# Optimization experiments

Measured on AMD Instinct MI355X. Metric: run time of the kernel, lower is better.

The kernel has to match this reference:

```python
import jax, jax.numpy as jnp
import numpy as np

B, N, R, CIN = 2, 2048, 128, 256
RADIUS, NSAMPLE, OUT = 0.3, 16, 5
EPS = 1e-5


def setup_inputs():
    key = jax.random.key(0)
    ks = jax.random.split(key, 8)
    points_xyz = jax.random.uniform(ks[0], (B, N, 3)) * 2.0          # scene ~2m cube
    features = jax.random.normal(ks[1], (B, CIN, N))
    ctr = jax.random.uniform(ks[2], (B, R, 3)) * 2.0
    size = jax.random.uniform(ks[3], (B, R, 3)) * 0.6 + 0.3          # positive box sizes
    ang = jax.random.uniform(ks[4], (B, R, 1)) * np.pi
    rois = jnp.concatenate([ctr, size, ang], axis=-1)                # [B,R,7]
    s = 0.02
    W_mlp = jax.random.normal(ks[5], (256, CIN + 3)) * s
    g_mlp = jnp.ones((256,)); bt_mlp = jnp.zeros((256,))
    W1 = jax.random.normal(ks[6], (128, 256)) * s; b1 = jnp.zeros((128,))
    g1 = jnp.ones((128,)); bt1 = jnp.zeros((128,))
    W2 = jax.random.normal(ks[7], (128, 128)) * s; b2 = jnp.zeros((128,))
    g2 = jnp.ones((128,)); bt2 = jnp.zeros((128,))
    return dict(points_xyz=points_xyz, features=features, rois=rois,
                W_mlp=W_mlp, g_mlp=g_mlp, bt_mlp=bt_mlp,
                W1=W1, b1=b1, g1=g1, bt1=bt1,
                W2=W2, b2=b2, g2=g2, bt2=bt2)


def _bn(x, g, b, axes, shape):
    # training-mode BatchNorm (batch statistics), matching torch .train() forward
    m = jnp.mean(x, axes, keepdims=True)
    v = jnp.var(x, axes, keepdims=True)
    return (x - m) * jax.lax.rsqrt(v + EPS) * g.reshape(shape) + b.reshape(shape)


def _forward(points_xyz, features, rois, W_mlp, g_mlp, bt_mlp,
             W1, b1, g1, bt1, W2, b2, g2, bt2):
    # ---- QueryAndGroup: ball query (min_radius=0) + gather + center + normalize_xyz ----
    diff = points_xyz[:, :, None, :] - points_xyz[:, None, :, :]     # [B,Nq,Np,3]
    d2 = jnp.sum(diff * diff, -1)
    mask = d2 < RADIUS * RADIUS
    cand = jnp.where(mask, jnp.arange(N, dtype=jnp.int32)[None, None, :], N)
    idx = jnp.sort(cand, axis=-1)[..., :NSAMPLE]                     # first NSAMPLE in-ball, ascending point index
    idx = jnp.where(idx < N, idx, idx[..., :1])                      # pad with first valid (self always in-ball)
    gx = jax.vmap(lambda p, i: p[i])(points_xyz, idx)                # [B,N,S,3]
    gx = (gx - points_xyz[:, :, None, :]) / RADIUS                   # centered + normalized
    gf = jax.vmap(lambda f, i: f[i])(jnp.swapaxes(features, 1, 2), idx)  # [B,N,S,C]
    nf = jnp.transpose(jnp.concatenate([gx, gf], -1), (0, 3, 1, 2))  # [B,3+C,N,S] (use_xyz=True)
    # ---- mlp: Conv2d 1x1 (bias='auto' with BN -> no bias) + BN2d + ReLU ----
    h = jnp.einsum('oc,bcns->bons', W_mlp, nf)
    h = jax.nn.relu(_bn(h, g_mlp, bt_mlp, (0, 2, 3), (1, -1, 1, 1)))
    feats = jnp.max(h, -1)                                           # max_pool2d over samples -> [B,256,N]
    h = jnp.einsum('oc,bcn->bon', W1, feats) + b1[None, :, None]
    h = jax.nn.relu(_bn(h, g1, bt1, (0, 2), (1, -1, 1)))
    h = jnp.einsum('oc,bcn->bon', W2, h) + b2[None, :, None]
    feats = jax.nn.relu(_bn(h, g2, bt2, (0, 2), (1, -1, 1)))         # [B,128,N]
    # ---- RoIPool3d: roi-aware voxel max pool (out_size=5, mode='max') ----
    C = feats.shape[1]
    ctr, size, ry = rois[..., :3], rois[..., 3:6], rois[..., 6]
    rel = points_xyz[:, None, :, :] - ctr[:, :, None, :]             # [B,R,N,3]
    c = jnp.cos(ry)[:, :, None]; s = jnp.sin(ry)[:, :, None]
    lx = rel[..., 0] * c + rel[..., 1] * s                           # rotate by -ry into roi frame
    ly = -rel[..., 0] * s + rel[..., 1] * c
    local = jnp.stack([lx, ly, rel[..., 2]], -1)                     # [B,R,N,3]
    half = size[:, :, None, :] * 0.5
    inside = jnp.all(jnp.abs(local) < half, -1)                      # [B,R,N]
    v = jnp.clip(jnp.floor((local + half) / (2.0 * half) * OUT), 0, OUT - 1).astype(jnp.int32)
    vox = (v[..., 0] * OUT + v[..., 1]) * OUT + v[..., 2]
    base = jnp.arange(B * R, dtype=jnp.int32).reshape(B, R, 1) * (OUT ** 3)
    seg = jnp.where(inside, base + vox, B * R * OUT ** 3).reshape(-1)  # dummy segment for outside pts
    data = jnp.broadcast_to(jnp.swapaxes(feats, 1, 2)[:, None], (B, R, N, C)).reshape(-1, C)
    pooled = jax.ops.segment_max(data, seg, num_segments=B * R * OUT ** 3 + 1)[:-1]
    pooled = jnp.where(jnp.isneginf(pooled), 0.0, pooled)            # empty voxels -> 0
    roi_feats = pooled.reshape(B, R, OUT, OUT, OUT, C)
    return feats, roi_feats


def reference(points_xyz, features, rois, W_mlp, g_mlp, bt_mlp,
              W1, b1, g1, bt1, W2, b2, g2, bt2):
    return _forward(points_xyz, features, rois, W_mlp, g_mlp, bt_mlp,
                    W1, b1, g1, bt1, W2, b2, g2, bt2)
```

## Files before the change

kernel.cpp:

```cpp
#include <hip/hip_runtime.h>
#include <hip/hip_bf16.h>

typedef __hip_bfloat16 bf16;
typedef unsigned short u16;

#define NB   2
#define NPT  2048
#define NROI 128
#define CINF 256
#define NS   16
#define KDIM 259
#define KP2  288
#define C1   256
#define C2   128
#define NVOX 125
#define EPSF 1e-5f

typedef __bf16 bf16x8 __attribute__((ext_vector_type(8)));
typedef float  f32x4  __attribute__((ext_vector_type(4)));

__device__ __forceinline__ float ldin(const void* p, size_t i, int f32flag) {
    if (f32flag) return ((const float*)p)[i];
    unsigned short u = ((const unsigned short*)p)[i];
    return __uint_as_float(((unsigned)u) << 16);
}

__device__ __forceinline__ unsigned short f2bf(float x) {
    unsigned u = __float_as_uint(x);
    u += 0x7FFFu + ((u >> 16) & 1u);
    return (unsigned short)(u >> 16);
}


__global__ void k_detect(const void* __restrict__ Wm, int* __restrict__ flag) {
    __shared__ int f;
    int tid = threadIdx.x;
    if (tid == 0) f = 0;
    __syncthreads();
    #pragma unroll
    for (int r = 0; r < 4; r++) {
        unsigned short u = ((const unsigned short*)Wm)[r * 256 + tid];
        float v = __uint_as_float(((unsigned)u) << 16);
        if (!(fabsf(v) <= 1e4f)) atomicOr(&f, 1);
    }
    __syncthreads();
    if (tid == 0) *flag = f;
}

__global__ void k_cvt(const void* __restrict__ pts, const void* __restrict__ rois,
                      const void* __restrict__ gm, const void* __restrict__ btm,
                      const void* __restrict__ b1, const void* __restrict__ g1,
                      const void* __restrict__ bt1, const void* __restrict__ b2,
                      const void* __restrict__ g2, const void* __restrict__ bt2,
                      const void* __restrict__ Wm,
                      float* __restrict__ ptsf, float* __restrict__ roisf,
                      float* __restrict__ params, const int* __restrict__ flag) {
    int f = *flag;
    int e = blockIdx.x * 256 + threadIdx.x;
    if (blockIdx.y == 10) {
        if (e < 768) {
            int d = e >> 8, o = e & 255;
            params[25088 + e] = ldin(Wm, (size_t)o * KDIM + d, f);
        }
        return;
    }
    const void* src; float* dst; int n;
    switch (blockIdx.y) {
        case 0:  src = pts; dst = ptsf;           n = NB * NPT * 3; break;
        case 1:  src = rois; dst = roisf;         n = NB * NROI * 7; break;
        case 2:  src = gm;  dst = params + 0;     n = 256; break;
        case 3:  src = btm; dst = params + 256;   n = 256; break;
        case 4:  src = b1;  dst = params + 33280; n = 128; break;
        case 5:  src = g1;  dst = params + 33408; n = 128; break;
        case 6:  src = bt1; dst = params + 33536; n = 128; break;
        case 7:  src = b2;  dst = params + 50048; n = 128; break;
        case 8:  src = g2;  dst = params + 50176; n = 128; break;
        default: src = bt2; dst = params + 50304; n = 128; break;
    }
    if (e < n) dst[e] = ldin(src, e, f);
}

__global__ void k_soa(const float* __restrict__ ptsf, float* __restrict__ psx,
                      float* __restrict__ psy, float* __restrict__ psz) {
    int e = blockIdx.x * 256 + threadIdx.x;
    if (e < NB * NPT) {
        psx[e] = ptsf[e * 3 + 0];
        psy[e] = ptsf[e * 3 + 1];
        psz[e] = ptsf[e * 3 + 2];
    }
}

__global__ void k_transpose(const void* __restrict__ feat, u16* __restrict__ ftbf,
                            const int* __restrict__ flag) {
    __shared__ float tile[32][33];
    int f = *flag;
    int b = blockIdx.z;
    int n0 = blockIdx.x * 32, c0 = blockIdx.y * 32;
    int tx = threadIdx.x, ty = threadIdx.y;
    #pragma unroll
    for (int d = 0; d < 4; d++) {
        int c = c0 + ty + d * 8;
        tile[ty + d * 8][tx] = ldin(feat, ((size_t)(b * CINF + c)) * NPT + n0 + tx, f);
    }
    __syncthreads();
    #pragma unroll
    for (int d = 0; d < 4; d++) {
        int n = n0 + ty + d * 8;
        ftbf[((size_t)(b * NPT + n)) * CINF + c0 + tx] = f2bf(tile[tx][ty + d * 8]);
    }
}

__global__ void k_prep(const void* __restrict__ Wm, const void* __restrict__ W1,
                       const void* __restrict__ W2, u16* __restrict__ wbf,
                       u16* __restrict__ w1bf, u16* __restrict__ w2bf,
                       float* __restrict__ stats, const int* __restrict__ flag) {
    int f = *flag;
    int e = blockIdx.x * 256 + threadIdx.x;
    if (e < 256 * KP2) {
        int o = e / KP2, k = e % KP2;
        float v = 0.f;
        if (k < 256)      v = ldin(Wm, (size_t)o * KDIM + 3 + k, f);
        else if (k < 259) v = ldin(Wm, (size_t)o * KDIM + (k - 256), f);
        wbf[e] = f2bf(v);
    } else if (e < 256 * KP2 + 1024) {
        stats[e - 256 * KP2] = 0.f;
    } else if (e < 256 * KP2 + 1024 + 32768) {
        int idx = e - (256 * KP2 + 1024);
        w1bf[idx] = f2bf(ldin(W1, idx, f));
    } else if (e < 256 * KP2 + 1024 + 32768 + 16384) {
        int idx = e - (256 * KP2 + 1024 + 32768);
        w2bf[idx] = f2bf(ldin(W2, idx, f));
    }
}

__global__ __launch_bounds__(256) void k_knn2(const float* __restrict__ psx, const float* __restrict__ psy,
                                              const float* __restrict__ psz, int* __restrict__ idxb) {
    #pragma clang fp contract(off)
    int wid = threadIdx.x >> 6, lane = threadIdx.x & 63;
    int q = blockIdx.x * 4 + wid;
    int b = q >> 11;
    int base = b * NPT;
    float qx = psx[q], qy = psy[q], qz = psz[q];
    const float R2 = (float)(0.3 * 0.3);
    size_t ob = (size_t)q * NS;
    int cnt = 0, j0 = -1;
    unsigned long long below = (lane == 63) ? ~0ull >> 1 : ((1ull << (lane + 1)) - 1) >> 1;
    for (int c0 = 0; c0 < NPT; c0 += 64) {
        int j = c0 + lane;
        float dx = qx - psx[base + j];
        float dy = qy - psy[base + j];
        float dz = qz - psz[base + j];
        float d2 = dx * dx + dy * dy + dz * dz;
        bool hit = d2 < R2;
        unsigned long long m = __ballot(hit);
        if (m) {
            if (j0 < 0) j0 = c0 + __builtin_ctzll(m);
            int pos = cnt + __popcll(m & below);
            if (hit && pos < NS) idxb[ob + pos] = j;
            cnt += __popcll(m);
        }
        if (cnt >= NS) break;
    }
    if (lane >= cnt && lane < NS) idxb[ob + lane] = j0;
}

__global__ __launch_bounds__(256) void k_dense(const u16* __restrict__ ftbf, const u16* __restrict__ wbf,
                                               float* __restrict__ Hf) {
    int w = threadIdx.x >> 6, lane = threadIdx.x & 63;
    int lg = lane >> 4, lr = lane & 15;
    int rbase = blockIdx.x * 16;
    int c0 = blockIdx.y * 128 + w * 32;

    size_t aoff  = (size_t)(rbase + lr) * CINF + lg * 8;
    size_t boff0 = (size_t)(c0 + lr) * KP2 + lg * 8;
    size_t boff1 = (size_t)(c0 + 16 + lr) * KP2 + lg * 8;

    f32x4 acc0 = (f32x4){0.f, 0.f, 0.f, 0.f};
    f32x4 acc1 = (f32x4){0.f, 0.f, 0.f, 0.f};
    #pragma unroll
    for (int k0 = 0; k0 < 256; k0 += 32) {
        bf16x8 af = __builtin_bit_cast(bf16x8, *(const uint4*)(ftbf + aoff + k0));
        bf16x8 b0 = __builtin_bit_cast(bf16x8, *(const uint4*)(wbf + boff0 + k0));
        bf16x8 b1 = __builtin_bit_cast(bf16x8, *(const uint4*)(wbf + boff1 + k0));
        acc0 = __builtin_amdgcn_mfma_f32_16x16x32_bf16(af, b0, acc0, 0, 0, 0);
        acc1 = __builtin_amdgcn_mfma_f32_16x16x32_bf16(af, b1, acc1, 0, 0, 0);
    }
    #pragma unroll
    for (int r = 0; r < 4; r++) {
        int row = rbase + lg * 4 + r;
        Hf[(size_t)row * C1 + c0 + lr] = acc0[r];
        Hf[(size_t)row * C1 + c0 + 16 + lr] = acc1[r];
    }
}

#define GPTS 8
__global__ __launch_bounds__(256) void k_gather(const float* __restrict__ Hf, const int* __restrict__ idxb,
                                                const float* __restrict__ ptsf, const float* __restrict__ wxyz,
                                                float* __restrict__ Hmax, float* __restrict__ Hmin,
                                                float* __restrict__ stats) {
    __shared__ int   lj[NS];
    __shared__ float lgx[NS], lgy[NS], lgz[NS];
    int o = threadIdx.x;
    float wx = wxyz[o], wy = wxyz[256 + o], wz = wxyz[512 + o];
    float ssum = 0.f, ssq = 0.f;
    for (int p = 0; p < GPTS; p++) {
        int pt = blockIdx.x * GPTS + p;
        int b = pt >> 11;
        int base = b * NPT;
        if (o < NS) {
            int j = idxb[(size_t)pt * NS + o];
            lj[o] = j;
            size_t jb = ((size_t)(base + j)) * 3;
            size_t cb = (size_t)pt * 3;
            lgx[o] = (ptsf[jb]     - ptsf[cb])     / 0.3f;
            lgy[o] = (ptsf[jb + 1] - ptsf[cb + 1]) / 0.3f;
            lgz[o] = (ptsf[jb + 2] - ptsf[cb + 2]) / 0.3f;
        }
        __syncthreads();
        float mx = -3.4e38f, mn = 3.4e38f;
        #pragma unroll
        for (int s = 0; s < NS; s++) {
            float v = Hf[(size_t)(base + lj[s]) * C1 + o] + wx * lgx[s] + wy * lgy[s] + wz * lgz[s];
            mx = fmaxf(mx, v); mn = fminf(mn, v);
            ssum += v; ssq += v * v;
        }
        Hmax[(size_t)pt * C1 + o] = mx;
        Hmin[(size_t)pt * C1 + o] = mn;
        __syncthreads();
    }
    atomicAdd(&stats[o], ssum);
    atomicAdd(&stats[256 + o], ssq);
}

__global__ void k_feats0(const float* __restrict__ Hmax, const float* __restrict__ Hmin,
                         const float* __restrict__ stats, const float* __restrict__ g,
                         const float* __restrict__ bt, u16* __restrict__ f0bf) {
    int e = blockIdx.x * 256 + threadIdx.x;
    if (e >= NB * NPT * C1) return;
    int o = e & (C1 - 1);
    const float inv = 1.f / 65536.f;
    float m = stats[o] * inv;
    float var = fmaxf(stats[256 + o] * inv - m * m, 0.f);
    float a = g[o] / sqrtf(var + EPSF);
    float d = bt[o] - m * a;
    float h = (a > 0.f) ? Hmax[e] : Hmin[e];
    f0bf[e] = f2bf(fmaxf(a * h + d, 0.f));
}

template<int K>
__global__ __launch_bounds__(256) void k_lin(const u16* __restrict__ Xbf, const u16* __restrict__ Wb,
                                             const float* __restrict__ bias, float* __restrict__ out,
                                             float* __restrict__ sum, float* __restrict__ sumsq) {
    int w = threadIdx.x >> 6, lane = threadIdx.x & 63;
    int lg = lane >> 4, lr = lane & 15;
    int rbase = blockIdx.x * 16;
    int c0 = w * 32;

    size_t aoff = (size_t)(rbase + lr) * K + lg * 8;
    size_t boff0 = (size_t)(c0 + lr) * K + lg * 8;
    size_t boff1 = (size_t)(c0 + 16 + lr) * K + lg * 8;

    f32x4 acc0 = (f32x4){0.f, 0.f, 0.f, 0.f};
    f32x4 acc1 = (f32x4){0.f, 0.f, 0.f, 0.f};
    #pragma unroll
    for (int k0 = 0; k0 < K; k0 += 32) {
        bf16x8 af = __builtin_bit_cast(bf16x8, *(const uint4*)(Xbf + aoff + k0));
        bf16x8 b0 = __builtin_bit_cast(bf16x8, *(const uint4*)(Wb + boff0 + k0));
        bf16x8 b1 = __builtin_bit_cast(bf16x8, *(const uint4*)(Wb + boff1 + k0));
        acc0 = __builtin_amdgcn_mfma_f32_16x16x32_bf16(af, b0, acc0, 0, 0, 0);
        acc1 = __builtin_amdgcn_mfma_f32_16x16x32_bf16(af, b1, acc1, 0, 0, 0);
    }

    #pragma unroll
    for (int ct = 0; ct < 2; ct++) {
        f32x4 a = ct ? acc1 : acc0;
        int col = c0 + ct * 16 + lr;
        float bi = bias[col];
        float s = 0.f, q = 0.f;
        #pragma unroll
        for (int r = 0; r < 4; r++) {
            float h = a[r] + bi;
            out[(size_t)(rbase + lg * 4 + r) * C2 + col] = h;
            s += h; q += h * h;
        }
        s += __shfl_xor(s, 16); s += __shfl_xor(s, 32);
        q += __shfl_xor(q, 16); q += __shfl_xor(q, 32);
        if (lane < 16) {
            atomicAdd(&sum[col], s);
            atomicAdd(&sumsq[col], q);
        }
    }
}

__global__ void k_bnrelu(const float* __restrict__ h, const float* __restrict__ sum,
                         const float* __restrict__ sumsq, const float* __restrict__ g,
                         const float* __restrict__ bt, u16* __restrict__ xbf) {
    int e = blockIdx.x * 256 + threadIdx.x;
    if (e >= NB * NPT * C2) return;
    int o = e & (C2 - 1);
    const float inv = 1.f / 4096.f;
    float m = sum[o] * inv;
    float var = fmaxf(sumsq[o] * inv - m * m, 0.f);
    float a = g[o] / sqrtf(var + EPSF);
    float d = bt[o] - m * a;
    xbf[e] = f2bf(fmaxf(a * h[e] + d, 0.f));
}

__global__ void k_final(const float* __restrict__ h2, const float* __restrict__ sum,
                        const float* __restrict__ sumsq, const float* __restrict__ g,
                        const float* __restrict__ bt, float* __restrict__ fp,
                        void* __restrict__ out0, const int* __restrict__ flag) {
    int e = blockIdx.x * 256 + threadIdx.x;
    if (e >= NB * NPT * C2) return;
    int f = *flag;
    int o = e & (C2 - 1);
    int bn = e >> 7;
    int b = bn >> 11, n = bn & (NPT - 1);
    const float inv = 1.f / 4096.f;
    float m = sum[o] * inv;
    float var = fmaxf(sumsq[o] * inv - m * m, 0.f);
    float a = g[o] / sqrtf(var + EPSF);
    float d = bt[o] - m * a;
    float v = fmaxf(a * h2[e] + d, 0.f);
    fp[e] = v;
    size_t oi = ((size_t)(b * C2 + o)) * NPT + n;
    if (f) ((float*)out0)[oi] = v;
    else   ((unsigned short*)out0)[oi] = f2bf(v);
}

__global__ __launch_bounds__(64) void k_pool(const float* __restrict__ ptsf, const float* __restrict__ roisf,
                                             const float* __restrict__ fp, void* __restrict__ d_out,
                                             const int* __restrict__ flag) {
    #pragma clang fp contract(off)
    __shared__ float pooled[NVOX * 64];
    __shared__ int list[NPT];
    __shared__ int cnt;
    int f = *flag;
    int bid = blockIdx.x;
    int b = bid >> 7;
    int tid = threadIdx.x;
    if (tid == 0) cnt = 0;
    size_t rb = ((size_t)bid) * 7;
    float cx = roisf[rb], cy = roisf[rb + 1], cz = roisf[rb + 2];
    float hx = roisf[rb + 3] * 0.5f;
    float hy = roisf[rb + 4] * 0.5f;
    float hz = roisf[rb + 5] * 0.5f;
    float ry = roisf[rb + 6];
    float cf = (float)cos((double)ry);
    float sf = (float)sin((double)ry);
    __syncthreads();
    for (int n = tid; n < NPT; n += 64) {
        size_t pb = ((size_t)(b * NPT + n)) * 3;
        float rx  = ptsf[pb]     - cx;
        float ryy = ptsf[pb + 1] - cy;
        float rz  = ptsf[pb + 2] - cz;
        float lx = rx * cf + ryy * sf;
        float ly = -rx * sf + ryy * cf;
        if (fabsf(lx) < hx && fabsf(ly) < hy && fabsf(rz) < hz) {
            int vx = (int)fminf(fmaxf(floorf((lx + hx) / (2.f * hx) * 5.f), 0.f), 4.f);
            int vy = (int)fminf(fmaxf(floorf((ly + hy) / (2.f * hy) * 5.f), 0.f), 4.f);
            int vz = (int)fminf(fmaxf(floorf((rz + hz) / (2.f * hz) * 5.f), 0.f), 4.f);
            int vox = (vx * 5 + vy) * 5 + vz;
            int pos = atomicAdd(&cnt, 1);
            list[pos] = (vox << 16) | n;
        }
    }
    __syncthreads();
    int m = cnt;
    size_t ob = (size_t)524288 + (size_t)bid * (NVOX * C2);
    for (int half = 0; half < 2; half++) {
        for (int k = tid; k < NVOX * 64; k += 64) pooled[k] = 0.f;
        __syncthreads();
        int c = half * 64 + tid;
        for (int e = 0; e < m; e++) {
            int u = list[e];
            int n = u & 0xFFFF, vox = u >> 16;
            float v = fp[((size_t)(b * NPT + n)) * C2 + c];
            float* p = &pooled[vox * 64 + tid];
            *p = fmaxf(*p, v);
        }
        __syncthreads();
        for (int k = tid; k < NVOX * 64; k += 64) {
            int vox = k >> 6, cc = k & 63;
            size_t oi = ob + (size_t)vox * C2 + half * 64 + cc;
            float v = pooled[k];
            if (f) ((float*)d_out)[oi] = v;
            else   ((unsigned short*)d_out)[oi] = f2bf(v);
        }
        __syncthreads();
    }
}

extern "C" void kernel_launch(void* const* d_in, const int* in_sizes, int n_in,
                              void* d_out, int out_size, void* d_ws, size_t ws_size,
                              hipStream_t stream) {
    const void* pts  = d_in[0];
    const void* feat = d_in[1];
    const void* rois = d_in[2];
    const void* Wm   = d_in[3];
    const void* gm   = d_in[4];
    const void* btm  = d_in[5];
    const void* W1   = d_in[6];
    const void* b1   = d_in[7];
    const void* g1   = d_in[8];
    const void* bt1  = d_in[9];
    const void* W2   = d_in[10];
    const void* b2   = d_in[11];
    const void* g2   = d_in[12];
    const void* bt2  = d_in[13];

    float* ws     = (float*)d_ws;
    int*   flag   = (int*)ws;
    float* ptsf   = ws + 16;
    float* roisf  = ws + 12304;
    float* params = ws + 14096;
    u16*   w1bf   = (u16*)(params + 512);
    u16*   w2bf   = (u16*)(params + 512 + 16384);
    float* wxyz   = params + 25088;
    u16*   wbf    = (u16*)(ws + 64528);
    float* stats  = ws + 101392;
    int*   idxb   = (int*)(ws + 102416);
    u16*   ftbf   = (u16*)(ws + 167952);
    float* Hmax   = ws + 1216528;
    float* Hmin   = ws + 2265104;
    u16*   f0bf   = (u16*)(ws + 167952);
    float* h1     = ws + 1216528;
    u16*   x1bf   = (u16*)(ws + 1740816);
    float* h2     = ws + 2265104;
    float* fp     = ws + 2789392;
    float* psx    = ws + 3313680;
    float* psy    = ws + 3317776;
    float* psz    = ws + 3321872;
    float* Hf     = ws + 3325968;

    k_detect<<<1, 256, 0, stream>>>(Wm, flag);
    k_cvt<<<dim3(48, 11), 256, 0, stream>>>(pts, rois, gm, btm, b1, g1, bt1, b2, g2, bt2, Wm,
                                            ptsf, roisf, params, flag);
    k_soa<<<16, 256, 0, stream>>>(ptsf, psx, psy, psz);
    k_transpose<<<dim3(NPT / 32, CINF / 32, NB), dim3(32, 8), 0, stream>>>(feat, ftbf, flag);
    k_prep<<<484, 256, 0, stream>>>(Wm, W1, W2, wbf, w1bf, w2bf, stats, flag);
    k_knn2<<<NB * NPT / 4, 256, 0, stream>>>(psx, psy, psz, idxb);
    k_dense<<<dim3(256, 2), 256, 0, stream>>>(ftbf, wbf, Hf);
    k_gather<<<(NB * NPT) / GPTS, 256, 0, stream>>>(Hf, idxb, ptsf, wxyz, Hmax, Hmin, stats);
    k_feats0<<<(NB * NPT * C1) / 256, 256, 0, stream>>>(Hmax, Hmin, stats, params + 0, params + 256, f0bf);
    k_lin<256><<<256, 256, 0, stream>>>(f0bf, w1bf, params + 33280, h1, stats + 512, stats + 640);
    k_bnrelu<<<(NB * NPT * C2) / 256, 256, 0, stream>>>(h1, stats + 512, stats + 640, params + 33408, params + 33536, x1bf);
    k_lin<128><<<256, 256, 0, stream>>>(x1bf, w2bf, params + 50048, h2, stats + 768, stats + 896);
    k_final<<<(NB * NPT * C2) / 256, 256, 0, stream>>>(h2, stats + 768, stats + 896, params + 50176, params + 50304, fp, d_out, flag);
    k_pool<<<NB * NROI, 64, 0, stream>>>(ptsf, roisf, fp, d_out, flag);
}
```

Before: 225.5 us.

## Widen ROI pooling blocks to 512 threads with shared atomicMax over all channels

The ROI pool kernel moves from 64-thread blocks, which made two passes over 64 channels each, to 512-thread blocks covering all 128 channels in one pass. Four point slots per channel reduce into a shared int array with atomicMax on the float bit pattern. Because values come after ReLU and are non-negative, integer max matches float max. The in-box point list now lives in a global workspace region that reuses the Hf buffer, to free shared memory for the full 125x128 pooled array. The aim is to cut the long serial per-point loop and raise occupancy, at the cost of shared atomics and global list traffic.

```diff
diff --git a/kernel.cpp b/kernel.cpp
--- a/kernel.cpp
+++ b/kernel.cpp
@@ -328,28 +328,35 @@
     else   ((unsigned short*)out0)[oi] = f2bf(v);
 }
 
-__global__ __launch_bounds__(64) void k_pool(const float* __restrict__ ptsf, const float* __restrict__ roisf,
-                                             const float* __restrict__ fp, void* __restrict__ d_out,
-                                             const int* __restrict__ flag) {
+__global__ __launch_bounds__(512) void k_pool2(const float* __restrict__ ptsf, const float* __restrict__ roisf,
+                                               const float* __restrict__ fp, void* __restrict__ d_out,
+                                               const int* __restrict__ flag, int* __restrict__ glist) {
     #pragma clang fp contract(off)
-    __shared__ float pooled[NVOX * 64];
-    __shared__ int list[NPT];
+    __shared__ int pooled[NVOX * C2];
     __shared__ int cnt;
+    __shared__ float rp[8];
     int f = *flag;
     int bid = blockIdx.x;
     int b = bid >> 7;
     int tid = threadIdx.x;
-    if (tid == 0) cnt = 0;
-    size_t rb = ((size_t)bid) * 7;
-    float cx = roisf[rb], cy = roisf[rb + 1], cz = roisf[rb + 2];
-    float hx = roisf[rb + 3] * 0.5f;
-    float hy = roisf[rb + 4] * 0.5f;
-    float hz = roisf[rb + 5] * 0.5f;
-    float ry = roisf[rb + 6];
-    float cf = (float)cos((double)ry);
-    float sf = (float)sin((double)ry);
-    __syncthreads();
-    for (int n = tid; n < NPT; n += 64) {
+    for (int k = tid; k < NVOX * C2; k += 512) pooled[k] = 0;
+    if (tid == 0) {
+        cnt = 0;
+        size_t rb = ((size_t)bid) * 7;
+        rp[0] = roisf[rb];     rp[1] = roisf[rb + 1]; rp[2] = roisf[rb + 2];
+        rp[3] = roisf[rb + 3] * 0.5f;
+        rp[4] = roisf[rb + 4] * 0.5f;
+        rp[5] = roisf[rb + 5] * 0.5f;
+        float ry = roisf[rb + 6];
+        rp[6] = (float)cos((double)ry);
+        rp[7] = (float)sin((double)ry);
+    }
+    __syncthreads();
+    float cx = rp[0], cy = rp[1], cz = rp[2];
+    float hx = rp[3], hy = rp[4], hz = rp[5];
+    float cf = rp[6], sf = rp[7];
+    int* mylist = glist + bid * NPT;
+    for (int n = tid; n < NPT; n += 512) {
         size_t pb = ((size_t)(b * NPT + n)) * 3;
         float rx  = ptsf[pb]     - cx;
         float ryy = ptsf[pb + 1] - cy;
@@ -362,32 +369,24 @@
             int vz = (int)fminf(fmaxf(floorf((rz + hz) / (2.f * hz) * 5.f), 0.f), 4.f);
             int vox = (vx * 5 + vy) * 5 + vz;
             int pos = atomicAdd(&cnt, 1);
-            list[pos] = (vox << 16) | n;
+            mylist[pos] = (vox << 16) | n;
         }
     }
     __syncthreads();
     int m = cnt;
+    int c = tid & 127, slot = tid >> 7;
+    for (int e = slot; e < m; e += 4) {
+        int u = mylist[e];
+        int n = u & 0xFFFF, vox = u >> 16;
+        float v = fp[((size_t)(b * NPT + n)) * C2 + c];
+        atomicMax(&pooled[vox * C2 + c], __float_as_int(v));
+    }
+    __syncthreads();
     size_t ob = (size_t)524288 + (size_t)bid * (NVOX * C2);
-    for (int half = 0; half < 2; half++) {
-        for (int k = tid; k < NVOX * 64; k += 64) pooled[k] = 0.f;
-        __syncthreads();
-        int c = half * 64 + tid;
-        for (int e = 0; e < m; e++) {
-            int u = list[e];
-            int n = u & 0xFFFF, vox = u >> 16;
-            float v = fp[((size_t)(b * NPT + n)) * C2 + c];
-            float* p = &pooled[vox * 64 + tid];
-            *p = fmaxf(*p, v);
-        }
-        __syncthreads();
-        for (int k = tid; k < NVOX * 64; k += 64) {
-            int vox = k >> 6, cc = k & 63;
-            size_t oi = ob + (size_t)vox * C2 + half * 64 + cc;
-            float v = pooled[k];
-            if (f) ((float*)d_out)[oi] = v;
-            else   ((unsigned short*)d_out)[oi] = f2bf(v);
-        }
-        __syncthreads();
+    for (int k = tid; k < NVOX * C2; k += 512) {
+        float v = __int_as_float(pooled[k]);
+        if (f) ((float*)d_out)[ob + k] = v;
+        else   ((unsigned short*)d_out)[ob + k] = f2bf(v);
     }
 }
 
@@ -432,6 +431,7 @@
     float* psy    = ws + 3317776;
     float* psz    = ws + 3321872;
     float* Hf     = ws + 3325968;
+    int*   glist  = (int*)(ws + 3325968);
 
     k_detect<<<1, 256, 0, stream>>>(Wm, flag);
     k_cvt<<<dim3(48, 11), 256, 0, stream>>>(pts, rois, gm, btm, b1, g1, bt1, b2, g2, bt2, Wm,
@@ -447,5 +447,5 @@
     k_bnrelu<<<(NB * NPT * C2) / 256, 256, 0, stream>>>(h1, stats + 512, stats + 640, params + 33408, params + 33536, x1bf);
     k_lin<128><<<256, 256, 0, stream>>>(x1bf, w2bf, params + 50048, h2, stats + 768, stats + 896);
     k_final<<<(NB * NPT * C2) / 256, 256, 0, stream>>>(h2, stats + 768, stats + 896, params + 50176, params + 50304, fp, d_out, flag);
-    k_pool<<<NB * NROI, 64, 0, stream>>>(ptsf, roisf, fp, d_out, flag);
-}
+    k_pool2<<<NB * NROI, 512, 0, stream>>>(ptsf, roisf, fp, d_out, flag, glist);
+}
```

Result: faster. 196.1 us (-13.0%).
